# Optimization experiments

Hardware: AMD Instinct MI355X
Metric: run time of the kernel (lower is better)

## Reference

```python
import jax, jax.numpy as jnp
import numpy as np
from jax import lax

G = 8        # group_num
BS = 32      # blocksize
SC = 13      # sample_channel = round(32*32*0.1/8)


def conv2d(x, w, b=None, stride=1, pad=0):
    y = lax.conv_general_dilated(x, w, (stride, stride), [(pad, pad), (pad, pad)],
                                 dimension_numbers=("NCHW", "OIHW", "NCHW"))
    if b is not None:
        y = y + b[None, :, None, None]
    return y


def prelu(x, a):
    return jnp.where(x >= 0, x, a * x)


def depth_to_space(x, bs):
    # matches Reshape_Concat_Adap: channel index = c_out*bs*bs + i*bs + j
    b, c, h, w = x.shape
    co = c // (bs * bs)
    x = x.reshape(b, co, bs, bs, h, w)
    x = x.transpose(0, 1, 4, 2, 5, 3)  # b, co, h, bs, w, bs
    return x.reshape(b, co, h * bs, w * bs)


def setup_inputs() -> dict:
    key = jax.random.key(0)
    ks = jax.random.split(key, 16)
    s = 0.05
    inp = {
        "x": jax.random.normal(ks[0], (8, 1, 256, 256), jnp.float32),
        "sample_w": jax.random.normal(ks[1], (G, SC, 1, BS, BS), jnp.float32) * 0.02,
        "up_w": jax.random.normal(ks[2], (G, BS * BS, SC, 1, 1), jnp.float32) * s,
        "up_b": jnp.zeros((G, BS * BS), jnp.float32),
        "conv1_w": jax.random.normal(ks[3], (G, 64, 1, 3, 3), jnp.float32) * s,
        "conv1_b": jnp.zeros((G, 64), jnp.float32),
        "conv1_a": jnp.full((G,), 0.25, jnp.float32),
        "fus_w": jax.random.normal(ks[4], (G - 1, 64, 128, 3, 3), jnp.float32) * s,
        "fus_b": jnp.zeros((G - 1, 64), jnp.float32),
        "fus_a": jnp.full((G - 1,), 0.25, jnp.float32),
        "t2_w": jax.random.normal(ks[5], (G, 64, 64, 3, 3), jnp.float32) * s,
        "t2_b": jnp.zeros((G, 64), jnp.float32),
        "t2_a": jnp.full((G,), 0.25, jnp.float32),
        "t3_w": jax.random.normal(ks[6], (G, 64, 64, 3, 3), jnp.float32) * s,
        "t3_b": jnp.zeros((G, 64), jnp.float32),
        "t3_a": jnp.full((G,), 0.25, jnp.float32),
        "t4_w": jax.random.normal(ks[7], (G, 64, 64, 3, 3), jnp.float32) * s,
        "t4_b": jnp.zeros((G, 64), jnp.float32),
        "t4_a": jnp.full((G,), 0.25, jnp.float32),
        "t5_w": jax.random.normal(ks[8], (G, 1, 64, 3, 3), jnp.float32) * s,
        "t5_b": jnp.zeros((G, 1), jnp.float32),
    }
    return inp


def reference(x, sample_w, up_w, up_b, conv1_w, conv1_b, conv1_a,
              fus_w, fus_b, fus_a, t2_w, t2_b, t2_a, t3_w, t3_b, t3_a,
              t4_w, t4_b, t4_a, t5_w, t5_b):
    def head(g):
        y = conv2d(x, sample_w[g], stride=BS)              # [B,SC,H/32,W/32]
        y = conv2d(y, up_w[g], up_b[g])                    # [B,1024,H/32,W/32]
        y = depth_to_space(y, BS)                          # [B,1,H,W]
        return prelu(conv2d(y, conv1_w[g], conv1_b[g], pad=1), conv1_a[g])

    def tail(h, g):
        h = prelu(conv2d(h, t2_w[g], t2_b[g], pad=1), t2_a[g])
        h = prelu(conv2d(h, t3_w[g], t3_b[g], pad=1), t3_a[g])
        h = prelu(conv2d(h, t4_w[g], t4_b[g], pad=1), t4_a[g])
        return conv2d(h, t5_w[g], t5_b[g], pad=1)          # [B,1,H,W]

    heads = [head(g) for g in range(G)]
    cur = heads[0]
    outs = [tail(cur, 0)]
    for m in range(G - 1):
        cat = jnp.concatenate([cur, heads[m + 1]], axis=1)  # [B,128,H,W]
        cur = prelu(conv2d(cat, fus_w[m], fus_b[m], pad=1), fus_a[m])
        outs.append(tail(cur, m + 1))
    return jnp.stack(outs, axis=0)  # [G,B,1,H,W]
```

## Files before the change

### kernel.cpp

```cpp
#include <hip/hip_runtime.h>
#include <stdint.h>

typedef __attribute__((ext_vector_type(8))) short short8;
typedef __attribute__((ext_vector_type(16))) float floatx16;

#define PLANE 16777216

__device__ __forceinline__ float b2f(short s) {
  union { uint32_t u; float f; } v; v.u = ((uint32_t)(uint16_t)s) << 16; return v.f;
}
__device__ __forceinline__ short f2b(float f) {
  union { float f; uint32_t u; } v; v.f = f;
  uint32_t r = (v.u + 0x7FFFu + ((v.u >> 16) & 1u)) >> 16;
  return (short)r;
}

__device__ __forceinline__ uint32_t ldsAddr(int r, int xp, int c) {
  uint32_t byte = ((uint32_t)(r * 258 + xp) << 6) + ((uint32_t)c << 1);
  byte ^= ((uint32_t)(xp & 7)) << 4;
  return byte;
}

template<int NCHUNK>
__global__ __launch_bounds__(512, 2)
void k_conv(const short* __restrict__ in1, const short* __restrict__ in2,
            const short* __restrict__ wp, const float* __restrict__ bias,
            const float* __restrict__ alpha, short* __restrict__ out)
{
  __shared__ __align__(16) uint8_t smem[3 * 258 * 64];
  const int wg = blockIdx.x;
  const int b = wg & 7;
  const int y = wg >> 3;
  const int tid = threadIdx.x;
  const int l = tid & 63;
  const int w = tid >> 6;
  const int lm = l & 31;
  const int lh = l >> 5;

  floatx16 acc[2];
  #pragma unroll
  for (int nb = 0; nb < 2; ++nb)
    #pragma unroll
    for (int r = 0; r < 16; ++r) acc[nb][r] = 0.f;

  const int xbase = w * 32 + lm;

  short8 stg[6];

  auto issue = [&](int q) {
    const short* __restrict__ src = ((q < 2) ? in1 : in2) + (size_t)(q & 1) * PLANE;
    #pragma unroll
    for (int i = 0; i < 6; ++i) {
      int widx = tid + i * 512;
      int r = widx >> 10;
      int xp = ((widx >> 2) & 255) + 1;
      int co = (widx & 3) << 3;
      int yy = y + r - 1;
      short8 v = {0, 0, 0, 0, 0, 0, 0, 0};
      if ((unsigned)yy < 256u)
        v = *(const short8*)(src + ((b * 256 + yy) * 256 + (xp - 1)) * 32 + co);
      stg[i] = v;
    }
  };
  auto commit = [&]() {
    #pragma unroll
    for (int i = 0; i < 6; ++i) {
      int widx = tid + i * 512;
      int r = widx >> 10;
      int xp = ((widx >> 2) & 255) + 1;
      int co = (widx & 3) << 3;
      *(short8*)(smem + ldsAddr(r, xp, co)) = stg[i];
    }
  };

  if (tid < 24) {
    short8 z = {0, 0, 0, 0, 0, 0, 0, 0};
    int r = tid >> 3;
    int xp = (tid & 4) ? 257 : 0;
    int co = (tid & 3) << 3;
    *(short8*)(smem + ldsAddr(r, xp, co)) = z;
  }

  issue(0);
  commit();
  __syncthreads();

  #pragma unroll
  for (int q = 0; q < NCHUNK; ++q) {
    if (q + 1 < NCHUNK) issue(q + 1);

    __builtin_amdgcn_s_setprio(1);
    #pragma unroll
    for (int ky = 0; ky < 3; ++ky)
    #pragma unroll
    for (int kx = 0; kx < 3; ++kx)
    #pragma unroll
    for (int s = 0; s < 2; ++s) {
      const int ks = (q * 9 + ky * 3 + kx) * 2 + s;
      const short8 bw0 = *(const short8*)(wp + ((ks * 2 + 0) * 64 + l) * 8);
      const short8 bw1 = *(const short8*)(wp + ((ks * 2 + 1) * 64 + l) * 8);
      const int cl = s * 16 + lh * 8;
      const int xp = xbase + kx;
      const short8 av = *(const short8*)(smem + ldsAddr(ky, xp, cl));
      acc[0] = __builtin_amdgcn_mfma_f32_32x32x16_bf16(av, bw0, acc[0], 0, 0, 0);
      acc[1] = __builtin_amdgcn_mfma_f32_32x32x16_bf16(av, bw1, acc[1], 0, 0, 0);
    }
    __builtin_amdgcn_s_setprio(0);

    if (q + 1 < NCHUNK) {
      __syncthreads();
      commit();
      __syncthreads();
    }
  }

  const float alp = alpha[0];
  #pragma unroll
  for (int nb = 0; nb < 2; ++nb) {
    const float bs = bias[nb * 32 + lm];
    short* __restrict__ op = out + (size_t)nb * PLANE + lm;
    #pragma unroll
    for (int r = 0; r < 16; ++r) {
      int px = w * 32 + (r & 3) + ((r >> 2) << 3) + (lh << 2);
      float v = acc[nb][r] + bs;
      v = v >= 0.f ? v : alp * v;
      op[((b * 256 + y) * 256 + px) * 32] = f2b(v);
    }
  }
}

__global__ __launch_bounds__(256)
void k_pack(const float* __restrict__ w2, const float* __restrict__ w3,
            const float* __restrict__ w4, const float* __restrict__ wf,
            short* __restrict__ wp234, short* __restrict__ wpfus)
{
  int idx = blockIdx.x * 256 + threadIdx.x;
  if (idx < 24 * 36864) {
    int conv = idx / 36864;
    int r = idx - conv * 36864;
    int which = conv >> 3, g = conv & 7;
    const float* W = (which == 0 ? w2 : which == 1 ? w3 : w4) + g * 36864;
    int ks = r >> 10;
    int nblk = (r >> 9) & 1;
    int lane = (r >> 3) & 63;
    int e = r & 7;
    int q = ks / 18, tt = ks % 18;
    int t = tt >> 1, s = tt & 1;
    int cin = q * 32 + s * 16 + ((lane >> 5) << 3) + e;
    int cout = nblk * 32 + (lane & 31);
    int ky = t / 3, kx = t % 3;
    wp234[idx] = f2b(W[((cout * 64 + cin) * 3 + ky) * 3 + kx]);
  } else {
    int idx2 = idx - 24 * 36864;
    if (idx2 >= 7 * 73728) return;
    int conv = idx2 / 73728;
    int r = idx2 - conv * 73728;
    const float* W = wf + conv * 73728;
    int ks = r >> 10;
    int nblk = (r >> 9) & 1;
    int lane = (r >> 3) & 63;
    int e = r & 7;
    int q = ks / 18, tt = ks % 18;
    int t = tt >> 1, s = tt & 1;
    int cin = q * 32 + s * 16 + ((lane >> 5) << 3) + e;
    int cout = nblk * 32 + (lane & 31);
    int ky = t / 3, kx = t % 3;
    wpfus[idx2] = f2b(W[((cout * 128 + cin) * 3 + ky) * 3 + kx]);
  }
}

__global__ __launch_bounds__(256)
void k_sample(const float* __restrict__ x, const float* __restrict__ sw,
              float* __restrict__ s_all)
{
  int idx = blockIdx.x * 256 + threadIdx.x;
  int gx = idx & 7, gy = (idx >> 3) & 7;
  int t = idx >> 6;
  int c = t % 13; t /= 13;
  int b = t & 7, g = t >> 3;
  const float* xb = x + b * 65536 + (gy * 32) * 256 + gx * 32;
  const float* wp = sw + (g * 13 + c) * 1024;
  float acc = 0.f;
  for (int i = 0; i < 32; ++i) {
    #pragma unroll
    for (int j = 0; j < 32; ++j) acc += xb[i * 256 + j] * wp[i * 32 + j];
  }
  s_all[idx] = acc;
}

__global__ __launch_bounds__(256)
void k_upz(const float* __restrict__ s_all, const float* __restrict__ upw,
           const float* __restrict__ upb, float* __restrict__ z_all)
{
  int idx = blockIdx.x * 256 + threadIdx.x;
  int x = idx & 255, y = (idx >> 8) & 255;
  int b = (idx >> 16) & 7, g = idx >> 19;
  int pos = (y & 31) * 32 + (x & 31);
  int gy = y >> 5, gx = x >> 5;
  const float* sp = s_all + ((g * 8 + b) * 13) * 64 + gy * 8 + gx;
  const float* wp = upw + (g * 1024 + pos) * 13;
  float a = upb[g * 1024 + pos];
  #pragma unroll
  for (int c = 0; c < 13; ++c) a += wp[c] * sp[c * 64];
  z_all[idx] = a;
}

__global__ __launch_bounds__(256)
void k_conv1(const float* __restrict__ z, const float* __restrict__ w,
             const float* __restrict__ bias, const float* __restrict__ alpha,
             short* __restrict__ out)
{
  int wg = blockIdx.x;
  int b = wg & 7;
  int y = wg >> 3;
  int x = threadIdx.x;
  int pid = (b * 256 + y) * 256 + x;
  float zv[9];
  #pragma unroll
  for (int t = 0; t < 9; ++t) {
    int dy = t / 3, dx = t % 3;
    int yy = y + dy - 1, xx = x + dx - 1;
    zv[t] = ((unsigned)yy < 256u && (unsigned)xx < 256u)
              ? z[b * 65536 + yy * 256 + xx] : 0.f;
  }
  float alp = alpha[0];
  #pragma unroll
  for (int c0 = 0; c0 < 64; c0 += 8) {
    short8 pack;
    #pragma unroll
    for (int e = 0; e < 8; ++e) {
      int c = c0 + e;
      float a = bias[c];
      #pragma unroll
      for (int t = 0; t < 9; ++t) a += w[c * 9 + t] * zv[t];
      a = a >= 0.f ? a : alp * a;
      pack[e] = f2b(a);
    }
    *(short8*)(out + (size_t)(c0 >> 5) * PLANE + pid * 32 + (c0 & 31)) = pack;
  }
}

__global__ __launch_bounds__(256)
void k_t5(const short* __restrict__ in, const float* __restrict__ w,
          const float* __restrict__ bias, float* __restrict__ out)
{
  int wg = blockIdx.x;
  int b = wg & 7;
  int y = wg >> 3;
  int x = threadIdx.x;
  float acc = bias[0];
  for (int dy = 0; dy < 3; ++dy) {
    int yy = y + dy - 1;
    if ((unsigned)yy >= 256u) continue;
    for (int dx = 0; dx < 3; ++dx) {
      int xx = x + dx - 1;
      if ((unsigned)xx >= 256u) continue;
      const int pix = (b * 256 + yy) * 256 + xx;
      #pragma unroll
      for (int c0 = 0; c0 < 64; c0 += 8) {
        short8 v = *(const short8*)(in + (size_t)(c0 >> 5) * PLANE + pix * 32 + (c0 & 31));
        #pragma unroll
        for (int e = 0; e < 8; ++e)
          acc += w[(c0 + e) * 9 + dy * 3 + dx] * b2f(v[e]);
      }
    }
  }
  out[(b * 256 + y) * 256 + x] = acc;
}

extern "C" void kernel_launch(void* const* d_in, const int* in_sizes, int n_in,
                              void* d_out, int out_size, void* d_ws, size_t ws_size,
                              hipStream_t stream) {
  const float* X   = (const float*)d_in[0];
  const float* SW  = (const float*)d_in[1];
  const float* UPW = (const float*)d_in[2];
  const float* UPB = (const float*)d_in[3];
  const float* C1W = (const float*)d_in[4];
  const float* C1B = (const float*)d_in[5];
  const float* C1A = (const float*)d_in[6];
  const float* FW  = (const float*)d_in[7];
  const float* FB  = (const float*)d_in[8];
  const float* FA  = (const float*)d_in[9];
  const float* W2  = (const float*)d_in[10];
  const float* B2  = (const float*)d_in[11];
  const float* A2  = (const float*)d_in[12];
  const float* W3  = (const float*)d_in[13];
  const float* B3  = (const float*)d_in[14];
  const float* A3  = (const float*)d_in[15];
  const float* W4  = (const float*)d_in[16];
  const float* B4  = (const float*)d_in[17];
  const float* A4  = (const float*)d_in[18];
  const float* W5  = (const float*)d_in[19];
  const float* B5  = (const float*)d_in[20];
  float* OUT = (float*)d_out;
  (void)in_sizes; (void)n_in; (void)out_size; (void)ws_size;

  uint8_t* base = (uint8_t*)d_ws;
  size_t off = 0;
  auto alloc = [&](size_t bytes) -> uint8_t* {
    uint8_t* r = base + off;
    off += (bytes + 255) & ~(size_t)255;
    return r;
  };
  const size_t ACT_ELEMS = 2ull * PLANE;
  short* act[3];
  for (int i = 0; i < 3; ++i) act[i] = (short*)alloc(ACT_ELEMS * 2);
  float* z_all = (float*)alloc(4194304ull * 4);
  float* s_all = (float*)alloc(53248ull * 4);
  short* wp234 = (short*)alloc(884736ull * 2);
  short* wpfus = (short*)alloc(516096ull * 2);

  k_pack<<<dim3(5472), dim3(256), 0, stream>>>(W2, W3, W4, FW, wp234, wpfus);
  k_sample<<<dim3(208), dim3(256), 0, stream>>>(X, SW, s_all);
  k_upz<<<dim3(16384), dim3(256), 0, stream>>>(s_all, UPW, UPB, z_all);

  int cur = 0, A = 1, B = 2;
  k_conv1<<<dim3(2048), dim3(256), 0, stream>>>(z_all, C1W, C1B, C1A, act[cur]);

  for (int m = 0; m < 8; ++m) {
    const short* wp_t2 = wp234 + (0 * 8 + m) * 36864;
    const short* wp_t3 = wp234 + (1 * 8 + m) * 36864;
    const short* wp_t4 = wp234 + (2 * 8 + m) * 36864;

    k_conv<2><<<dim3(2048), dim3(512), 0, stream>>>(
        act[cur], act[cur], wp_t2, B2 + m * 64, A2 + m, act[A]);
    k_conv<2><<<dim3(2048), dim3(512), 0, stream>>>(
        act[A], act[A], wp_t3, B3 + m * 64, A3 + m, act[B]);
    k_conv<2><<<dim3(2048), dim3(512), 0, stream>>>(
        act[B], act[B], wp_t4, B4 + m * 64, A4 + m, act[A]);
    k_t5<<<dim3(2048), dim3(256), 0, stream>>>(
        act[A], W5 + m * 576, B5 + m, OUT + (size_t)m * 524288);

    if (m < 7) {
      k_conv1<<<dim3(2048), dim3(256), 0, stream>>>(
          z_all + (size_t)(m + 1) * 524288, C1W + (m + 1) * 576,
          C1B + (m + 1) * 64, C1A + (m + 1), act[B]);
      k_conv<4><<<dim3(2048), dim3(512), 0, stream>>>(
          act[cur], act[B], wpfus + m * 73728, FB + m * 64, FA + m, act[A]);
      int tmp = cur; cur = A; A = tmp;
    }
  }
}
```

Before: 2.908 ms.

## Switch activation layout to 16-channel planes with finer LDS chunking

Activations are re-laid out from 32-channel planes to 16-channel planes, so each conv stages 16 input channels per chunk instead of 32. This halves the LDS tile and the per-thread staging registers, and the LDS address swizzle is changed to suit the 32-byte row stride. The weight packing, conv1 and t5 kernels are updated to the new layout. In exchange, chunk count doubles, so twice as many barrier and commit phases run per conv. Output stores also become narrower-strided scalar writes.

New measurement: 2.666 ms. 1.09x faster.

```diff
diff --git a/kernel.cpp b/kernel.cpp
--- a/kernel.cpp
+++ b/kernel.cpp
@@ -4,7 +4,7 @@
 typedef __attribute__((ext_vector_type(8))) short short8;
 typedef __attribute__((ext_vector_type(16))) float floatx16;
 
-#define PLANE 16777216
+#define PLANE16 8388608
 
 __device__ __forceinline__ float b2f(short s) {
   union { uint32_t u; float f; } v; v.u = ((uint32_t)(uint16_t)s) << 16; return v.f;
@@ -15,19 +15,19 @@
   return (short)r;
 }
 
-__device__ __forceinline__ uint32_t ldsAddr(int r, int xp, int c) {
-  uint32_t byte = ((uint32_t)(r * 258 + xp) << 6) + ((uint32_t)c << 1);
-  byte ^= ((uint32_t)(xp & 7)) << 4;
+__device__ __forceinline__ uint32_t ldsA(int r, int xp, int c) {
+  uint32_t byte = ((uint32_t)(r * 258 + xp) << 5) + ((uint32_t)c << 1);
+  byte ^= (uint32_t)((((xp >> 2) ^ (xp >> 3) ^ (xp >> 4)) & 1) << 4);
   return byte;
 }
 
-template<int NCHUNK>
+template<int NC16>
 __global__ __launch_bounds__(512, 2)
 void k_conv(const short* __restrict__ in1, const short* __restrict__ in2,
             const short* __restrict__ wp, const float* __restrict__ bias,
             const float* __restrict__ alpha, short* __restrict__ out)
 {
-  __shared__ __align__(16) uint8_t smem[3 * 258 * 64];
+  __shared__ __align__(16) uint8_t smem[3 * 258 * 32];
   const int wg = blockIdx.x;
   const int b = wg & 7;
   const int y = wg >> 3;
@@ -45,40 +45,43 @@
 
   const int xbase = w * 32 + lm;
 
-  short8 stg[6];
-
-  auto issue = [&](int q) {
-    const short* __restrict__ src = ((q < 2) ? in1 : in2) + (size_t)(q & 1) * PLANE;
-    #pragma unroll
-    for (int i = 0; i < 6; ++i) {
+  short8 stg[3];
+
+  auto issue = [&](int c16) {
+    const short* __restrict__ src =
+        ((c16 < 4) ? in1 : in2) + (size_t)(c16 & 3) * PLANE16;
+    #pragma unroll
+    for (int i = 0; i < 3; ++i) {
       int widx = tid + i * 512;
-      int r = widx >> 10;
-      int xp = ((widx >> 2) & 255) + 1;
-      int co = (widx & 3) << 3;
+      int r = widx >> 9;
+      int rem = widx & 511;
+      int xp = (rem >> 1) + 1;
+      int half = rem & 1;
       int yy = y + r - 1;
       short8 v = {0, 0, 0, 0, 0, 0, 0, 0};
       if ((unsigned)yy < 256u)
-        v = *(const short8*)(src + ((b * 256 + yy) * 256 + (xp - 1)) * 32 + co);
+        v = *(const short8*)(src + ((b * 256 + yy) * 256 + (xp - 1)) * 16 + half * 8);
       stg[i] = v;
     }
   };
   auto commit = [&]() {
     #pragma unroll
-    for (int i = 0; i < 6; ++i) {
+    for (int i = 0; i < 3; ++i) {
       int widx = tid + i * 512;
-      int r = widx >> 10;
-      int xp = ((widx >> 2) & 255) + 1;
-      int co = (widx & 3) << 3;
-      *(short8*)(smem + ldsAddr(r, xp, co)) = stg[i];
+      int r = widx >> 9;
+      int rem = widx & 511;
+      int xp = (rem >> 1) + 1;
+      int half = rem & 1;
+      *(short8*)(smem + ldsA(r, xp, half * 8)) = stg[i];
     }
   };
 
-  if (tid < 24) {
+  if (tid < 12) {
     short8 z = {0, 0, 0, 0, 0, 0, 0, 0};
-    int r = tid >> 3;
-    int xp = (tid & 4) ? 257 : 0;
-    int co = (tid & 3) << 3;
-    *(short8*)(smem + ldsAddr(r, xp, co)) = z;
+    int r = tid >> 2;
+    int xp = (tid & 2) ? 257 : 0;
+    int half = tid & 1;
+    *(short8*)(smem + ldsA(r, xp, half * 8)) = z;
   }
 
   issue(0);
@@ -86,28 +89,26 @@
   __syncthreads();
 
   #pragma unroll
-  for (int q = 0; q < NCHUNK; ++q) {
-    if (q + 1 < NCHUNK) issue(q + 1);
+  for (int c16 = 0; c16 < NC16; ++c16) {
+    if (c16 + 1 < NC16) issue(c16 + 1);
 
     __builtin_amdgcn_s_setprio(1);
     #pragma unroll
     for (int ky = 0; ky < 3; ++ky)
     #pragma unroll
-    for (int kx = 0; kx < 3; ++kx)
-    #pragma unroll
-    for (int s = 0; s < 2; ++s) {
-      const int ks = (q * 9 + ky * 3 + kx) * 2 + s;
+    for (int kx = 0; kx < 3; ++kx) {
+      const int ks = c16 * 9 + ky * 3 + kx;
       const short8 bw0 = *(const short8*)(wp + ((ks * 2 + 0) * 64 + l) * 8);
       const short8 bw1 = *(const short8*)(wp + ((ks * 2 + 1) * 64 + l) * 8);
-      const int cl = s * 16 + lh * 8;
+      const int cl = lh * 8;
       const int xp = xbase + kx;
-      const short8 av = *(const short8*)(smem + ldsAddr(ky, xp, cl));
+      const short8 av = *(const short8*)(smem + ldsA(ky, xp, cl));
       acc[0] = __builtin_amdgcn_mfma_f32_32x32x16_bf16(av, bw0, acc[0], 0, 0, 0);
       acc[1] = __builtin_amdgcn_mfma_f32_32x32x16_bf16(av, bw1, acc[1], 0, 0, 0);
     }
     __builtin_amdgcn_s_setprio(0);
 
-    if (q + 1 < NCHUNK) {
+    if (c16 + 1 < NC16) {
       __syncthreads();
       commit();
       __syncthreads();
@@ -118,13 +119,13 @@
   #pragma unroll
   for (int nb = 0; nb < 2; ++nb) {
     const float bs = bias[nb * 32 + lm];
-    short* __restrict__ op = out + (size_t)nb * PLANE + lm;
+    short* __restrict__ op = out + (size_t)(nb * 2 + (lm >> 4)) * PLANE16 + (lm & 15);
     #pragma unroll
     for (int r = 0; r < 16; ++r) {
       int px = w * 32 + (r & 3) + ((r >> 2) << 3) + (lh << 2);
       float v = acc[nb][r] + bs;
       v = v >= 0.f ? v : alp * v;
-      op[((b * 256 + y) * 256 + px) * 32] = f2b(v);
+      op[((b * 256 + y) * 256 + px) * 16] = f2b(v);
     }
   }
 }
@@ -144,9 +145,9 @@
     int nblk = (r >> 9) & 1;
     int lane = (r >> 3) & 63;
     int e = r & 7;
-    int q = ks / 18, tt = ks % 18;
-    int t = tt >> 1, s = tt & 1;
-    int cin = q * 32 + s * 16 + ((lane >> 5) << 3) + e;
+    int c16 = ks / 9;
+    int t = ks - c16 * 9;
+    int cin = c16 * 16 + ((lane >> 5) << 3) + e;
     int cout = nblk * 32 + (lane & 31);
     int ky = t / 3, kx = t % 3;
     wp234[idx] = f2b(W[((cout * 64 + cin) * 3 + ky) * 3 + kx]);
@@ -160,9 +161,9 @@
     int nblk = (r >> 9) & 1;
     int lane = (r >> 3) & 63;
     int e = r & 7;
-    int q = ks / 18, tt = ks % 18;
-    int t = tt >> 1, s = tt & 1;
-    int cin = q * 32 + s * 16 + ((lane >> 5) << 3) + e;
+    int c16 = ks / 9;
+    int t = ks - c16 * 9;
+    int cin = c16 * 16 + ((lane >> 5) << 3) + e;
     int cout = nblk * 32 + (lane & 31);
     int ky = t / 3, kx = t % 3;
     wpfus[idx2] = f2b(W[((cout * 128 + cin) * 3 + ky) * 3 + kx]);
@@ -236,7 +237,7 @@
       a = a >= 0.f ? a : alp * a;
       pack[e] = f2b(a);
     }
-    *(short8*)(out + (size_t)(c0 >> 5) * PLANE + pid * 32 + (c0 & 31)) = pack;
+    *(short8*)(out + (size_t)(c0 >> 4) * PLANE16 + pid * 16 + (c0 & 8)) = pack;
   }
 }
 
@@ -258,7 +259,7 @@
       const int pix = (b * 256 + yy) * 256 + xx;
       #pragma unroll
       for (int c0 = 0; c0 < 64; c0 += 8) {
-        short8 v = *(const short8*)(in + (size_t)(c0 >> 5) * PLANE + pix * 32 + (c0 & 31));
+        short8 v = *(const short8*)(in + (size_t)(c0 >> 4) * PLANE16 + pix * 16 + (c0 & 8));
         #pragma unroll
         for (int e = 0; e < 8; ++e)
           acc += w[(c0 + e) * 9 + dy * 3 + dx] * b2f(v[e]);
@@ -302,7 +303,7 @@
     off += (bytes + 255) & ~(size_t)255;
     return r;
   };
-  const size_t ACT_ELEMS = 2ull * PLANE;
+  const size_t ACT_ELEMS = 4ull * PLANE16;
   short* act[3];
   for (int i = 0; i < 3; ++i) act[i] = (short*)alloc(ACT_ELEMS * 2);
   float* z_all = (float*)alloc(4194304ull * 4);
@@ -322,11 +323,11 @@
     const short* wp_t3 = wp234 + (1 * 8 + m) * 36864;
     const short* wp_t4 = wp234 + (2 * 8 + m) * 36864;
 
-    k_conv<2><<<dim3(2048), dim3(512), 0, stream>>>(
+    k_conv<4><<<dim3(2048), dim3(512), 0, stream>>>(
         act[cur], act[cur], wp_t2, B2 + m * 64, A2 + m, act[A]);
-    k_conv<2><<<dim3(2048), dim3(512), 0, stream>>>(
+    k_conv<4><<<dim3(2048), dim3(512), 0, stream>>>(
         act[A], act[A], wp_t3, B3 + m * 64, A3 + m, act[B]);
-    k_conv<2><<<dim3(2048), dim3(512), 0, stream>>>(
+    k_conv<4><<<dim3(2048), dim3(512), 0, stream>>>(
         act[B], act[B], wp_t4, B4 + m * 64, A4 + m, act[A]);
     k_t5<<<dim3(2048), dim3(256), 0, stream>>>(
         act[A], W5 + m * 576, B5 + m, OUT + (size_t)m * 524288);
@@ -335,7 +336,7 @@
       k_conv1<<<dim3(2048), dim3(256), 0, stream>>>(
           z_all + (size_t)(m + 1) * 524288, C1W + (m + 1) * 576,
           C1B + (m + 1) * 64, C1A + (m + 1), act[B]);
-      k_conv<4><<<dim3(2048), dim3(512), 0, stream>>>(
+      k_conv<8><<<dim3(2048), dim3(512), 0, stream>>>(
           act[cur], act[B], wpfus + m * 73728, FB + m * 64, FA + m, act[A]);
       int tmp = cur; cur = A; A = tmp;
     }
```
